# Kernel optimization log

Measured on AMD Instinct MI355X. Metric: run time of the kernel, lower is better.

Reference implementation:

```python
import jax, jax.numpy as jnp
import numpy as np

# Large negative stand-in for -inf so logaddexp gradients stay finite;
# exp(NEG - x) underflows to 0 exactly, matching the -inf math on the
# reachable alignment lattice.
NEG = -1e30

N_FRAMES, BATCH, TARGET_LEN, VOCAB = 2000, 32, 1000, 256


def _alignment_alphas(score_mat, tgt):
    """Monotonic-alignment DP for one item.

    score_mat: [N, V] log-probs, tgt: [T] int token ids.
    Recurrence (same math as compute_loss):
      alpha[0, 0] = score[0, tgt[0]];          alpha[0, j>0] = -inf
      alpha[i, 0] = alpha[i-1, 0] + score[i, tgt[0]]            (cumsum column 0)
      alpha[i, j] = score[i, tgt[j]] + logaddexp(alpha[i-1, j-1], alpha[i-1, j])
    Returns the full lattice alphas: [N, T].
    """
    emit = score_mat[:, tgt]  # [N, T] gather of per-frame target log-probs
    t = tgt.shape[0]
    alpha0 = jnp.where(jnp.arange(t) == 0, emit[0], NEG)

    def step(alpha, e):
        shifted = jnp.concatenate([jnp.full((1,), NEG, alpha.dtype), alpha[:-1]])
        # j=0: logaddexp(NEG, alpha[0]) == alpha[0] -> pure cumsum, as in torch code
        new = e + jnp.logaddexp(shifted, alpha)
        return new, new

    _, rest = jax.lax.scan(step, alpha0, emit[1:])
    return jnp.concatenate([alpha0[None, :], rest], axis=0)  # [N, T]


def setup_inputs() -> dict:
    key = jax.random.key(0)
    k1, k2, k3, k4 = jax.random.split(key, 4)
    logits = jax.random.normal(k1, (N_FRAMES, BATCH, VOCAB), dtype=jnp.float32)
    scores = jax.nn.log_softmax(logits, axis=-1)  # module expects log-softmaxed scores
    targets = jax.random.randint(k2, (BATCH, TARGET_LEN), 0, VOCAB)
    # valid alignments need target_len <= input_len
    input_lengths = jax.random.randint(k3, (BATCH,), N_FRAMES // 2, N_FRAMES + 1)
    target_lengths = jax.random.randint(k4, (BATCH,), TARGET_LEN // 2, TARGET_LEN + 1)
    return {
        "scores": scores,
        "targets": targets,
        "input_lengths": input_lengths,
        "target_lengths": target_lengths,
    }


def reference(scores, targets, input_lengths, target_lengths):
    sc = jnp.transpose(scores, (1, 0, 2))  # [B, N, V]
    alphas = jax.vmap(_alignment_alphas)(sc, targets)  # [B, N, T]
    b = targets.shape[0]
    final = alphas[jnp.arange(b), input_lengths - 1, target_lengths - 1]  # [B]
    return -jnp.sum(final) / b
```

## Files before the change

### kernel.cpp

```cpp
#include <hip/hip_runtime.h>
#include <hip/hip_fp16.h>

constexpr int N_FRAMES   = 2000;
constexpr int BATCH      = 32;
constexpr int TARGET_LEN = 1000;
constexpr int VOCAB      = 256;
constexpr int CH         = 16;
constexpr int NW         = 8;
#define NEGF (-1e30f)

typedef __attribute__((address_space(1))) const float* gcfp;
typedef __attribute__((address_space(1))) const unsigned* gcu32;

typedef float f32x2 __attribute__((ext_vector_type(2)));

#define H2F(us) __half2float(__ushort_as_half((unsigned short)(us)))

__device__ __forceinline__ f32x2 lse_e(f32x2 A, f32x2 U, f32x2 E) {
    f32x2 m; m.x = fmaxf(A.x, U.x); m.y = fmaxf(A.y, U.y);
    const f32x2 d = A - U;
    f32x2 x;
    x.x = __builtin_amdgcn_exp2f(-fabsf(d.x));
    x.y = __builtin_amdgcn_exp2f(-fabsf(d.y));
    const f32x2 s = E + m;
    f32x2 tt = x * 0.0464048f - 0.1963066f;
    tt = x * tt + 0.4176245f;
    tt = x * tt - 0.7096745f;
    tt = x * tt + 1.44196727f;
    return x * tt + s;
}
__device__ __forceinline__ f32x2 lse_core(f32x2 A, f32x2 U) {
    f32x2 m; m.x = fmaxf(A.x, U.x); m.y = fmaxf(A.y, U.y);
    const f32x2 d = A - U;
    f32x2 x;
    x.x = __builtin_amdgcn_exp2f(-fabsf(d.x));
    x.y = __builtin_amdgcn_exp2f(-fabsf(d.y));
    f32x2 tt = x * 0.0464048f - 0.1963066f;
    tt = x * tt + 0.4176245f;
    tt = x * tt - 0.7096745f;
    tt = x * tt + 1.44196727f;
    return x * tt + m;
}

__global__ __launch_bounds__(256)
void gather_emit(const float* __restrict__ scores,
                 const int*   __restrict__ targets,
                 __half*      __restrict__ emit)
{
    constexpr float L2E = 1.44269504088896340736f;
    const int i = blockIdx.x;
    const int b = blockIdx.y;
    const int t = threadIdx.x;

    const gcfp gsc = (gcfp)scores;
    const unsigned sbase = (unsigned)(i * BATCH * VOCAB + b * VOCAB);

    int tk0, tk1, tk2, tk3;
    if (t < TARGET_LEN / 4) {
        const int4 tk = *(const int4*)&targets[b * TARGET_LEN + 4 * t];
        tk0 = tk.x; tk1 = tk.y; tk2 = tk.z; tk3 = tk.w;
    } else {
        tk0 = tk1 = tk2 = tk3 = targets[b * TARGET_LEN + TARGET_LEN - 1];
    }

    const float e0 = gsc[sbase + (unsigned)tk0] * L2E;
    const float e1 = gsc[sbase + (unsigned)tk1] * L2E;
    const float e2 = gsc[sbase + (unsigned)tk2] * L2E;
    const float e3 = gsc[sbase + (unsigned)tk3] * L2E;

    const unsigned long long h0 = __half_as_ushort(__float2half_rn(e0));
    const unsigned long long h1 = __half_as_ushort(__float2half_rn(e1));
    const unsigned long long h2 = __half_as_ushort(__float2half_rn(e2));
    const unsigned long long h3 = __half_as_ushort(__float2half_rn(e3));

    const unsigned long long u = h0 | (h1 << 16) | (h2 << 32) | (h3 << 48);
    *(unsigned long long*)(emit + (((size_t)(b * N_FRAMES + i)) << 10) + 4 * t) = u;
}

__global__ __launch_bounds__(512)
void align_dp_fb(const __half* __restrict__ emit,
                 const int*    __restrict__ in_len,
                 const int*    __restrict__ tg_len,
                 float*        __restrict__ wsA,
                 float*        __restrict__ wsB)
{
    const int b    = blockIdx.x;
    const int t    = threadIdx.x;
    const int lane = t & 63;
    const int w    = t >> 6;

    __shared__ float bpub[NW - 1][2][CH];

    const int inlen = in_len[b];
    const int m     = (inlen - 1) >> 1;

    const gcu32 gem = (gcu32)(emit + (((size_t)b * N_FRAMES) << 10));

    if (blockIdx.y == 0) {
        const int NCHf = (m + CH - 1) / CH;
        float p0 = NEGF, p1 = NEGF;
        if (t == 0) p0 = H2F(gem[0] & 0xffffu);

        unsigned ring[CH];
#pragma unroll
        for (int r = 0; r < CH; ++r) ring[r] = gem[(unsigned)((1 + r) << 9) + (unsigned)t];

        float shprev = NEGF, carry = NEGF;
        f32x2* wsA2 = (f32x2*)(wsA + (b << 10));

#define FROWX(r, SNAPF, Bv, Ov)                                                 \
        {                                                                       \
            const int i = i0 + (r);                                             \
            const unsigned u = ring[r];                                         \
            ring[r] = gem[(unsigned)((i + CH) << 9) + (unsigned)t];             \
            f32x2 E; E.x = H2F(u & 0xffffu); E.y = H2F(u >> 16);                \
            f32x2 A; A.x = (lane == 0) ? (Bv) : shprev; A.y = p0;               \
            f32x2 U; U.x = p0; U.y = p1;                                        \
            const f32x2 c = lse_e(A, U, E);                                     \
            shprev = __shfl_up(c.y, 1);                                         \
            (Ov) = c.y;                                                         \
            if (SNAPF) { if (i == m) wsA2[t] = c; }                             \
            p0 = c.x; p1 = c.y;                                                 \
        }

#define FBODY(SNAPF)                                                            \
        {                                                                       \
            FROWX(0,  SNAPF, B0,  o0)  FROWX(1,  SNAPF, B1,  o1)                \
            FROWX(2,  SNAPF, B2,  o2)  FROWX(3,  SNAPF, B3,  o3)                \
            FROWX(4,  SNAPF, B4,  o4)  FROWX(5,  SNAPF, B5,  o5)                \
            FROWX(6,  SNAPF, B6,  o6)  FROWX(7,  SNAPF, B7,  o7)                \
            FROWX(8,  SNAPF, B8,  o8)  FROWX(9,  SNAPF, B9,  o9)                \
            FROWX(10, SNAPF, B10, o10) FROWX(11, SNAPF, B11, o11)               \
            FROWX(12, SNAPF, B12, o12) FROWX(13, SNAPF, B13, o13)               \
            FROWX(14, SNAPF, B14, o14) FROWX(15, SNAPF, B15, o15)               \
        }

        const int NPHf = NCHf + NW - 1;
        for (int p = 0; p < NPHf; ++p) {
            const int q = p - w;
            if (q >= 0 && q < NCHf) {
                const int i0  = 1 + q * CH;
                const int par = q & 1;

                float B0 = NEGF, B1 = NEGF, B2 = NEGF, B3 = NEGF,
                      B4 = NEGF, B5 = NEGF, B6 = NEGF, B7 = NEGF,
                      B8 = NEGF, B9 = NEGF, B10 = NEGF, B11 = NEGF,
                      B12 = NEGF, B13 = NEGF, B14 = NEGF, B15 = NEGF;
                if (w > 0) {
                    const float* vp = &bpub[w - 1][par][0];
                    B0 = carry;
                    B1  = vp[0];  B2  = vp[1];  B3  = vp[2];  B4  = vp[3];
                    B5  = vp[4];  B6  = vp[5];  B7  = vp[6];  B8  = vp[7];
                    B9  = vp[8];  B10 = vp[9];  B11 = vp[10]; B12 = vp[11];
                    B13 = vp[12]; B14 = vp[13]; B15 = vp[14];
                    carry = vp[15];
                }

                float o0, o1, o2, o3, o4, o5, o6, o7,
                      o8, o9, o10, o11, o12, o13, o14, o15;

                if (q == NCHf - 1) FBODY(true) else FBODY(false)

                if (w < NW - 1 && lane == 63) {
                    float* dp = &bpub[w][par][0];
                    dp[0]  = o0;  dp[1]  = o1;  dp[2]  = o2;  dp[3]  = o3;
                    dp[4]  = o4;  dp[5]  = o5;  dp[6]  = o6;  dp[7]  = o7;
                    dp[8]  = o8;  dp[9]  = o9;  dp[10] = o10; dp[11] = o11;
                    dp[12] = o12; dp[13] = o13; dp[14] = o14; dp[15] = o15;
                }
            }
            asm volatile("s_waitcnt lgkmcnt(0)" ::: "memory");
            __builtin_amdgcn_s_barrier();
            asm volatile("" ::: "memory");
        }
#undef FBODY
#undef FROWX
    } else {
        const int tlen   = tg_len[b];
        const int istart = inlen - 1;
        const int NCHb   = (istart - m + CH - 1) / CH;
        const int fth    = (tlen - 1) >> 1;
        const int fcc    = (tlen - 1) & 1;

        float p0 = NEGF, p1 = NEGF;
        if (t == fth) { if (fcc == 0) p0 = 0.0f; else p1 = 0.0f; }

        unsigned ring[CH];
#pragma unroll
        for (int r = 0; r < CH; ++r)
            ring[r] = gem[(unsigned)((istart - r) << 9) + (unsigned)t];

        f32x2* wsB2 = (f32x2*)(wsB + (b << 10));

#define BROWX(r, SNAPF, Bv, Ov)                                                 \
        {                                                                       \
            const int i = i0 - (r);                                             \
            const unsigned u = ring[r];                                         \
            ring[r] = gem[(unsigned)((i + 1 - CH) << 9) + (unsigned)t];         \
            f32x2 E; E.x = H2F(u & 0xffffu); E.y = H2F(u >> 16);                \
            f32x2 P; P.x = p0; P.y = p1;                                        \
            const f32x2 x = E + P;                                              \
            const float sh = __shfl_down(x.x, 1);                               \
            (Ov) = x.x;                                                         \
            const float xR = (lane == 63) ? (Bv) : sh;                          \
            f32x2 A; A.x = x.x; A.y = x.y;                                      \
            f32x2 U; U.x = x.y; U.y = xR;                                       \
            const f32x2 c = lse_core(A, U);                                     \
            if (SNAPF) { if (i == m) wsB2[t] = c; }                             \
            p0 = c.x; p1 = c.y;                                                 \
        }

#define BBODY(SNAPF)                                                            \
        {                                                                       \
            BROWX(0,  SNAPF, B0,  o0)  BROWX(1,  SNAPF, B1,  o1)                \
            BROWX(2,  SNAPF, B2,  o2)  BROWX(3,  SNAPF, B3,  o3)                \
            BROWX(4,  SNAPF, B4,  o4)  BROWX(5,  SNAPF, B5,  o5)                \
            BROWX(6,  SNAPF, B6,  o6)  BROWX(7,  SNAPF, B7,  o7)                \
            BROWX(8,  SNAPF, B8,  o8)  BROWX(9,  SNAPF, B9,  o9)                \
            BROWX(10, SNAPF, B10, o10) BROWX(11, SNAPF, B11, o11)               \
            BROWX(12, SNAPF, B12, o12) BROWX(13, SNAPF, B13, o13)               \
            BROWX(14, SNAPF, B14, o14) BROWX(15, SNAPF, B15, o15)               \
        }

        const int NPHb = NCHb + NW - 1;
        for (int p = 0; p < NPHb; ++p) {
            const int q = p - (NW - 1 - w);
            if (q >= 0 && q < NCHb) {
                const int i0  = istart - 1 - q * CH;
                const int par = q & 1;

                float B0 = NEGF, B1 = NEGF, B2 = NEGF, B3 = NEGF,
                      B4 = NEGF, B5 = NEGF, B6 = NEGF, B7 = NEGF,
                      B8 = NEGF, B9 = NEGF, B10 = NEGF, B11 = NEGF,
                      B12 = NEGF, B13 = NEGF, B14 = NEGF, B15 = NEGF;
                if (w < NW - 1) {
                    const float* vp = &bpub[w][par][0];
                    B0  = vp[0];  B1  = vp[1];  B2  = vp[2];  B3  = vp[3];
                    B4  = vp[4];  B5  = vp[5];  B6  = vp[6];  B7  = vp[7];
                    B8  = vp[8];  B9  = vp[9];  B10 = vp[10]; B11 = vp[11];
                    B12 = vp[12]; B13 = vp[13]; B14 = vp[14]; B15 = vp[15];
                }

                float o0, o1, o2, o3, o4, o5, o6, o7,
                      o8, o9, o10, o11, o12, o13, o14, o15;

                if (q == NCHb - 1) BBODY(true) else BBODY(false)

                if (w > 0 && lane == 0) {
                    float* dp = &bpub[w - 1][par][0];
                    dp[0]  = o0;  dp[1]  = o1;  dp[2]  = o2;  dp[3]  = o3;
                    dp[4]  = o4;  dp[5]  = o5;  dp[6]  = o6;  dp[7]  = o7;
                    dp[8]  = o8;  dp[9]  = o9;  dp[10] = o10; dp[11] = o11;
                    dp[12] = o12; dp[13] = o13; dp[14] = o14; dp[15] = o15;
                }
            }
            asm volatile("s_waitcnt lgkmcnt(0)" ::: "memory");
            __builtin_amdgcn_s_barrier();
            asm volatile("" ::: "memory");
        }
#undef BBODY
#undef BROWX
    }
}

__global__ __launch_bounds__(512)
void lse_combine(const float* __restrict__ wsA, const float* __restrict__ wsB,
                 float* __restrict__ ws_final)
{
    constexpr float LN2 = 0.69314718055994530942f;
    const int b = blockIdx.x, t = threadIdx.x, lane = t & 63, w = t >> 6;
    __shared__ float red[8];

    const float* A  = wsA + (b << 10);
    const float* Bv = wsB + (b << 10);
    const float v0 = A[2 * t]     + Bv[2 * t];
    const float v1 = A[2 * t + 1] + Bv[2 * t + 1];

    float mx = fmaxf(v0, v1);
#pragma unroll
    for (int off = 1; off < 64; off <<= 1) mx = fmaxf(mx, __shfl_xor(mx, off));
    if (lane == 0) red[w] = mx;
    __syncthreads();
    float gm = red[0];
#pragma unroll
    for (int k = 1; k < 8; ++k) gm = fmaxf(gm, red[k]);

    float s = __builtin_amdgcn_exp2f(v0 - gm) + __builtin_amdgcn_exp2f(v1 - gm);
#pragma unroll
    for (int off = 1; off < 64; off <<= 1) s += __shfl_xor(s, off);
    __syncthreads();
    if (lane == 0) red[w] = s;
    __syncthreads();
    if (t == 0) {
        float tot = red[0];
#pragma unroll
        for (int k = 1; k < 8; ++k) tot += red[k];
        ws_final[b] = (gm + __builtin_amdgcn_logf(tot)) * LN2;
    }
}

__global__ void reduce_kernel(const float* __restrict__ ws_final, float* __restrict__ out)
{
    if (threadIdx.x == 0 && blockIdx.x == 0) {
        float s = 0.0f;
        for (int b = 0; b < BATCH; ++b) s += ws_final[b];
        out[0] = -s / (float)BATCH;
    }
}

#define CELL(dst, A, U, E)                                            \
    {                                                                 \
        const float m_ = fmaxf((A), (U));                             \
        const float d_ = (A) - (U);                                   \
        const float p_ = __builtin_amdgcn_exp2f(-fabsf(d_));          \
        const float l_ = __builtin_amdgcn_logf(1.0f + p_);            \
        (dst) = fmaf((E), L2E, m_ + l_);                              \
    }

__global__ __launch_bounds__(256)
void align_dp4(const float* __restrict__ scores,
               const int*   __restrict__ targets,
               const int*   __restrict__ in_len,
               const int*   __restrict__ tg_len,
               float*       __restrict__ ws_final)
{
    constexpr float L2E = 1.44269504088896340736f;
    constexpr float LN2 = 0.69314718055994530942f;

    const int b    = blockIdx.x;
    const int t    = threadIdx.x;
    const int lane = t & 63;
    const int w    = t >> 6;

    __shared__ float elds[4][VOCAB];
    __shared__ float bnd[2][8];

    const int inlen = in_len[b];
    const int tlen  = tg_len[b];

    const gcfp gsc = (gcfp)scores;
    const unsigned base = (unsigned)(b * VOCAB);
    constexpr unsigned ROWW = (unsigned)(BATCH * VOCAB);

    int tok[4];
#pragma unroll
    for (int c = 0; c < 4; ++c) {
        const int col = t * 4 + c;
        tok[c] = targets[b * TARGET_LEN + (col < TARGET_LEN ? col : TARGET_LEN - 1)];
    }

    float prev[4];
#pragma unroll
    for (int c = 0; c < 4; ++c) prev[c] = NEGF;
    if (t == 0) prev[0] = gsc[base + (unsigned)tok[0]] * L2E;

    elds[1][t] = gsc[1u * ROWW + base + (unsigned)t];
    elds[2][t] = gsc[2u * ROWW + base + (unsigned)t];
    if (lane == 63) bnd[0][w] = NEGF;

    float g[4];
    g[3] = gsc[3u * ROWW + base + (unsigned)t];
    g[0] = gsc[4u * ROWW + base + (unsigned)t];
    g[1] = gsc[5u * ROWW + base + (unsigned)t];
    g[2] = gsc[6u * ROWW + base + (unsigned)t];

    const int fth = (tlen - 1) >> 2;
    const int fcc = (tlen - 1) & 3;

#define STEP(K)                                                                    \
    {                                                                              \
        const int i = ib + (K);                                                    \
        if (i < N_FRAMES) {                                                        \
            asm volatile("s_waitcnt lgkmcnt(0)" ::: "memory");                     \
            __builtin_amdgcn_s_barrier();                                          \
            asm volatile("" ::: "memory");                                         \
            const int sl = i & 3;                                                  \
            const float ec0 = elds[sl][tok[0]];                                    \
            const float ec1 = elds[sl][tok[1]];                                    \
            const float ec2 = elds[sl][tok[2]];                                    \
            const float ec3 = elds[sl][tok[3]];                                    \
            const float fromLds = (w > 0) ? bnd[(i - 1) & 1][w - 1] : NEGF;        \
            if (i + 2 < N_FRAMES) elds[(i + 2) & 3][t] = g[((K) + 3) & 3];         \
            if (i + 6 < N_FRAMES)                                                  \
                g[((K) + 3) & 3] = gsc[(unsigned)(i + 6) * ROWW + base + (unsigned)t]; \
            const float sh   = __shfl_up(prev[3], 1);                              \
            const float left = (lane == 0) ? fromLds : sh;                         \
            float cur0, cur1, cur2, cur3;                                          \
            CELL(cur0, left,    prev[0], ec0);                                     \
            CELL(cur1, prev[0], prev[1], ec1);                                     \
            CELL(cur2, prev[1], prev[2], ec2);                                     \
            CELL(cur3, prev[2], prev[3], ec3);                                     \
            if (lane == 63) bnd[i & 1][w] = cur3;                                  \
            if (i == inlen - 1 && t == fth) {                                      \
                const float v = (fcc == 0) ? cur0 : (fcc == 1) ? cur1              \
                              : (fcc == 2) ? cur2 : cur3;                          \
                ws_final[b] = v * LN2;                                             \
            }                                                                      \
            prev[0] = cur0; prev[1] = cur1; prev[2] = cur2; prev[3] = cur3;        \
        }                                                                          \
    }

    for (int ib = 1; ib < N_FRAMES; ib += 4) {
        STEP(0) STEP(1) STEP(2) STEP(3)
    }
#undef STEP
}

extern "C" void kernel_launch(void* const* d_in, const int* in_sizes, int n_in,
                              void* d_out, int out_size, void* d_ws, size_t ws_size,
                              hipStream_t stream)
{
    const float* scores  = (const float*)d_in[0];
    const int*   targets = (const int*)  d_in[1];
    const int*   in_len  = (const int*)  d_in[2];
    const int*   tg_len  = (const int*)  d_in[3];
    float*       out     = (float*)d_out;
    float*       ws_fin  = (float*)d_ws;

    const size_t emit_bytes = (size_t)BATCH * N_FRAMES * 1024 * sizeof(__half);
    const size_t wsA_off  = 4096;
    const size_t wsB_off  = wsA_off + (size_t)BATCH * 1024 * sizeof(float);
    const size_t emit_off = wsB_off + (size_t)BATCH * 1024 * sizeof(float);
    const size_t need = emit_off + emit_bytes;

    if (ws_size >= need) {
        __half* emit = (__half*)((char*)d_ws + emit_off);
        float*  wsA  = (float*)((char*)d_ws + wsA_off);
        float*  wsB  = (float*)((char*)d_ws + wsB_off);
        dim3 ggrid(N_FRAMES, BATCH);
        gather_emit<<<ggrid, 256, 0, stream>>>(scores, targets, emit);
        align_dp_fb<<<dim3(BATCH, 2), 512, 0, stream>>>(emit, in_len, tg_len, wsA, wsB);
        lse_combine<<<BATCH, 512, 0, stream>>>(wsA, wsB, ws_fin);
    } else {
        align_dp4<<<BATCH, 256, 0, stream>>>(scores, targets, in_len, tg_len, ws_fin);
    }
    reduce_kernel<<<1, 64, 0, stream>>>(ws_fin, out);
}
```

Before: 202.7 us.

## Double DP chunk size, use Estrin log-polynomial, skip gather past input length

Raises the row chunk per wavefront phase from 16 to 32, which halves the number of barrier-synchronised phases and deepens the prefetch ring. The log2(1+x) polynomial is rewritten in Estrin form to shorten its dependency chain on the serial critical path. The gather kernel now returns early for frames at or beyond each item's input length, so it skips writing emissions that are never read. The larger chunk raises register pressure and lengthens pipeline fill and drain across the 8 wavefronts.

```diff
diff --git a/kernel.cpp b/kernel.cpp
--- a/kernel.cpp
+++ b/kernel.cpp
@@ -5,7 +5,7 @@
 constexpr int BATCH      = 32;
 constexpr int TARGET_LEN = 1000;
 constexpr int VOCAB      = 256;
-constexpr int CH         = 16;
+constexpr int CH         = 32;
 constexpr int NW         = 8;
 #define NEGF (-1e30f)
 
@@ -16,6 +16,15 @@
 
 #define H2F(us) __half2float(__ushort_as_half((unsigned short)(us)))
 
+__device__ __forceinline__ f32x2 l21p(f32x2 x) {
+    const f32x2 x2 = x * x;
+    const f32x2 x4 = x2 * x2;
+    f32x2 lo = x * 1.44196727f;
+    const f32x2 Bq = x * 0.4176245f  - 0.7096745f;
+    const f32x2 Cq = x * 0.0464048f  - 0.1963066f;
+    lo = x2 * Bq + lo;
+    return x4 * Cq + lo;
+}
 __device__ __forceinline__ f32x2 lse_e(f32x2 A, f32x2 U, f32x2 E) {
     f32x2 m; m.x = fmaxf(A.x, U.x); m.y = fmaxf(A.y, U.y);
     const f32x2 d = A - U;
@@ -23,11 +32,7 @@
     x.x = __builtin_amdgcn_exp2f(-fabsf(d.x));
     x.y = __builtin_amdgcn_exp2f(-fabsf(d.y));
     const f32x2 s = E + m;
-    f32x2 tt = x * 0.0464048f - 0.1963066f;
-    tt = x * tt + 0.4176245f;
-    tt = x * tt - 0.7096745f;
-    tt = x * tt + 1.44196727f;
-    return x * tt + s;
+    return l21p(x) + s;
 }
 __device__ __forceinline__ f32x2 lse_core(f32x2 A, f32x2 U) {
     f32x2 m; m.x = fmaxf(A.x, U.x); m.y = fmaxf(A.y, U.y);
@@ -35,21 +40,19 @@
     f32x2 x;
     x.x = __builtin_amdgcn_exp2f(-fabsf(d.x));
     x.y = __builtin_amdgcn_exp2f(-fabsf(d.y));
-    f32x2 tt = x * 0.0464048f - 0.1963066f;
-    tt = x * tt + 0.4176245f;
-    tt = x * tt - 0.7096745f;
-    tt = x * tt + 1.44196727f;
-    return x * tt + m;
+    return l21p(x) + m;
 }
 
 __global__ __launch_bounds__(256)
 void gather_emit(const float* __restrict__ scores,
                  const int*   __restrict__ targets,
+                 const int*   __restrict__ in_len,
                  __half*      __restrict__ emit)
 {
     constexpr float L2E = 1.44269504088896340736f;
     const int i = blockIdx.x;
     const int b = blockIdx.y;
+    if (i >= in_len[b]) return;
     const int t = threadIdx.x;
 
     const gcfp gsc = (gcfp)scores;
@@ -108,31 +111,20 @@
         float shprev = NEGF, carry = NEGF;
         f32x2* wsA2 = (f32x2*)(wsA + (b << 10));
 
-#define FROWX(r, SNAPF, Bv, Ov)                                                 \
-        {                                                                       \
-            const int i = i0 + (r);                                             \
+#define FBODY(SNAPF)                                                            \
+        _Pragma("unroll")                                                       \
+        for (int r = 0; r < CH; ++r) {                                          \
+            const int i = i0 + r;                                               \
             const unsigned u = ring[r];                                         \
             ring[r] = gem[(unsigned)((i + CH) << 9) + (unsigned)t];             \
             f32x2 E; E.x = H2F(u & 0xffffu); E.y = H2F(u >> 16);                \
-            f32x2 A; A.x = (lane == 0) ? (Bv) : shprev; A.y = p0;               \
+            f32x2 A; A.x = (lane == 0) ? Bv[r] : shprev; A.y = p0;              \
             f32x2 U; U.x = p0; U.y = p1;                                        \
             const f32x2 c = lse_e(A, U, E);                                     \
             shprev = __shfl_up(c.y, 1);                                         \
-            (Ov) = c.y;                                                         \
+            ov[r] = c.y;                                                        \
             if (SNAPF) { if (i == m) wsA2[t] = c; }                             \
             p0 = c.x; p1 = c.y;                                                 \
-        }
-
-#define FBODY(SNAPF)                                                            \
-        {                                                                       \
-            FROWX(0,  SNAPF, B0,  o0)  FROWX(1,  SNAPF, B1,  o1)                \
-            FROWX(2,  SNAPF, B2,  o2)  FROWX(3,  SNAPF, B3,  o3)                \
-            FROWX(4,  SNAPF, B4,  o4)  FROWX(5,  SNAPF, B5,  o5)                \
-            FROWX(6,  SNAPF, B6,  o6)  FROWX(7,  SNAPF, B7,  o7)                \
-            FROWX(8,  SNAPF, B8,  o8)  FROWX(9,  SNAPF, B9,  o9)                \
-            FROWX(10, SNAPF, B10, o10) FROWX(11, SNAPF, B11, o11)               \
-            FROWX(12, SNAPF, B12, o12) FROWX(13, SNAPF, B13, o13)               \
-            FROWX(14, SNAPF, B14, o14) FROWX(15, SNAPF, B15, o15)               \
         }
 
         const int NPHf = NCHf + NW - 1;
@@ -142,31 +134,23 @@
                 const int i0  = 1 + q * CH;
                 const int par = q & 1;
 
-                float B0 = NEGF, B1 = NEGF, B2 = NEGF, B3 = NEGF,
-                      B4 = NEGF, B5 = NEGF, B6 = NEGF, B7 = NEGF,
-                      B8 = NEGF, B9 = NEGF, B10 = NEGF, B11 = NEGF,
-                      B12 = NEGF, B13 = NEGF, B14 = NEGF, B15 = NEGF;
+                float Bv[CH], ov[CH];
+#pragma unroll
+                for (int r = 0; r < CH; ++r) Bv[r] = NEGF;
                 if (w > 0) {
                     const float* vp = &bpub[w - 1][par][0];
-                    B0 = carry;
-                    B1  = vp[0];  B2  = vp[1];  B3  = vp[2];  B4  = vp[3];
-                    B5  = vp[4];  B6  = vp[5];  B7  = vp[6];  B8  = vp[7];
-                    B9  = vp[8];  B10 = vp[9];  B11 = vp[10]; B12 = vp[11];
-                    B13 = vp[12]; B14 = vp[13]; B15 = vp[14];
-                    carry = vp[15];
+                    Bv[0] = carry;
+#pragma unroll
+                    for (int r = 1; r < CH; ++r) Bv[r] = vp[r - 1];
+                    carry = vp[CH - 1];
                 }
-
-                float o0, o1, o2, o3, o4, o5, o6, o7,
-                      o8, o9, o10, o11, o12, o13, o14, o15;
 
                 if (q == NCHf - 1) FBODY(true) else FBODY(false)
 
                 if (w < NW - 1 && lane == 63) {
                     float* dp = &bpub[w][par][0];
-                    dp[0]  = o0;  dp[1]  = o1;  dp[2]  = o2;  dp[3]  = o3;
-                    dp[4]  = o4;  dp[5]  = o5;  dp[6]  = o6;  dp[7]  = o7;
-                    dp[8]  = o8;  dp[9]  = o9;  dp[10] = o10; dp[11] = o11;
-                    dp[12] = o12; dp[13] = o13; dp[14] = o14; dp[15] = o15;
+#pragma unroll
+                    for (int r = 0; r < CH; ++r) dp[r] = ov[r];
                 }
             }
             asm volatile("s_waitcnt lgkmcnt(0)" ::: "memory");
@@ -174,7 +158,6 @@
             asm volatile("" ::: "memory");
         }
 #undef FBODY
-#undef FROWX
     } else {
         const int tlen   = tg_len[b];
         const int istart = inlen - 1;
@@ -192,17 +175,18 @@
 
         f32x2* wsB2 = (f32x2*)(wsB + (b << 10));
 
-#define BROWX(r, SNAPF, Bv, Ov)                                                 \
-        {                                                                       \
-            const int i = i0 - (r);                                             \
+#define BBODY(SNAPF)                                                            \
+        _Pragma("unroll")                                                       \
+        for (int r = 0; r < CH; ++r) {                                          \
+            const int i = i0 - r;                                               \
             const unsigned u = ring[r];                                         \
             ring[r] = gem[(unsigned)((i + 1 - CH) << 9) + (unsigned)t];         \
             f32x2 E; E.x = H2F(u & 0xffffu); E.y = H2F(u >> 16);                \
             f32x2 P; P.x = p0; P.y = p1;                                        \
             const f32x2 x = E + P;                                              \
             const float sh = __shfl_down(x.x, 1);                               \
-            (Ov) = x.x;                                                         \
-            const float xR = (lane == 63) ? (Bv) : sh;                          \
+            ov[r] = x.x;                                                        \
+            const float xR = (lane == 63) ? Bv[r] : sh;                         \
             f32x2 A; A.x = x.x; A.y = x.y;                                      \
             f32x2 U; U.x = x.y; U.y = xR;                                       \
             const f32x2 c = lse_core(A, U);                                     \
@@ -210,18 +194,6 @@
             p0 = c.x; p1 = c.y;                                                 \
         }
 
-#define BBODY(SNAPF)                                                            \
-        {                                                                       \
-            BROWX(0,  SNAPF, B0,  o0)  BROWX(1,  SNAPF, B1,  o1)                \
-            BROWX(2,  SNAPF, B2,  o2)  BROWX(3,  SNAPF, B3,  o3)                \
-            BROWX(4,  SNAPF, B4,  o4)  BROWX(5,  SNAPF, B5,  o5)                \
-            BROWX(6,  SNAPF, B6,  o6)  BROWX(7,  SNAPF, B7,  o7)                \
-            BROWX(8,  SNAPF, B8,  o8)  BROWX(9,  SNAPF, B9,  o9)                \
-            BROWX(10, SNAPF, B10, o10) BROWX(11, SNAPF, B11, o11)               \
-            BROWX(12, SNAPF, B12, o12) BROWX(13, SNAPF, B13, o13)               \
-            BROWX(14, SNAPF, B14, o14) BROWX(15, SNAPF, B15, o15)               \
-        }
-
         const int NPHb = NCHb + NW - 1;
         for (int p = 0; p < NPHb; ++p) {
             const int q = p - (NW - 1 - w);
@@ -229,29 +201,21 @@
                 const int i0  = istart - 1 - q * CH;
                 const int par = q & 1;
 
-                float B0 = NEGF, B1 = NEGF, B2 = NEGF, B3 = NEGF,
-                      B4 = NEGF, B5 = NEGF, B6 = NEGF, B7 = NEGF,
-                      B8 = NEGF, B9 = NEGF, B10 = NEGF, B11 = NEGF,
-                      B12 = NEGF, B13 = NEGF, B14 = NEGF, B15 = NEGF;
+                float Bv[CH], ov[CH];
+#pragma unroll
+                for (int r = 0; r < CH; ++r) Bv[r] = NEGF;
                 if (w < NW - 1) {
                     const float* vp = &bpub[w][par][0];
-                    B0  = vp[0];  B1  = vp[1];  B2  = vp[2];  B3  = vp[3];
-                    B4  = vp[4];  B5  = vp[5];  B6  = vp[6];  B7  = vp[7];
-                    B8  = vp[8];  B9  = vp[9];  B10 = vp[10]; B11 = vp[11];
-                    B12 = vp[12]; B13 = vp[13]; B14 = vp[14]; B15 = vp[15];
+#pragma unroll
+                    for (int r = 0; r < CH; ++r) Bv[r] = vp[r];
                 }
-
-                float o0, o1, o2, o3, o4, o5, o6, o7,
-                      o8, o9, o10, o11, o12, o13, o14, o15;
 
                 if (q == NCHb - 1) BBODY(true) else BBODY(false)
 
                 if (w > 0 && lane == 0) {
                     float* dp = &bpub[w - 1][par][0];
-                    dp[0]  = o0;  dp[1]  = o1;  dp[2]  = o2;  dp[3]  = o3;
-                    dp[4]  = o4;  dp[5]  = o5;  dp[6]  = o6;  dp[7]  = o7;
-                    dp[8]  = o8;  dp[9]  = o9;  dp[10] = o10; dp[11] = o11;
-                    dp[12] = o12; dp[13] = o13; dp[14] = o14; dp[15] = o15;
+#pragma unroll
+                    for (int r = 0; r < CH; ++r) dp[r] = ov[r];
                 }
             }
             asm volatile("s_waitcnt lgkmcnt(0)" ::: "memory");
@@ -259,7 +223,6 @@
             asm volatile("" ::: "memory");
         }
 #undef BBODY
-#undef BROWX
     }
 }
 
@@ -428,7 +391,7 @@
         float*  wsA  = (float*)((char*)d_ws + wsA_off);
         float*  wsB  = (float*)((char*)d_ws + wsB_off);
         dim3 ggrid(N_FRAMES, BATCH);
-        gather_emit<<<ggrid, 256, 0, stream>>>(scores, targets, emit);
+        gather_emit<<<ggrid, 256, 0, stream>>>(scores, targets, in_len, emit);
         align_dp_fb<<<dim3(BATCH, 2), 512, 0, stream>>>(emit, in_len, tg_len, wsA, wsB);
         lse_combine<<<BATCH, 512, 0, stream>>>(wsA, wsB, ws_fin);
     } else {
```

New measurement: 201.8 us. No clear change (-0.4%).

## Use DPP lane shifts, Estrin log polynomial, and skip gathers past input length

Applied to the files above, without the earlier changes.

Replaces the ds_bpermute-based shfl_up/shfl_down in the forward and backward DP inner loops with DPP row_shr/row_shl moves. The log2(1+x) polynomial is rewritten in Estrin form to shorten the dependency chain on the serial critical path. The gather kernel now exits early for frames beyond each item's input length, skipping unused emit writes. A risk is that DPP row shifts only operate within 16-lane rows, so lanes at row boundaries would receive 0 instead of their neighbour's value unless the bank/row masks handle it. That would break the wave-wide shift semantics.

```diff
diff --git a/kernel.cpp b/kernel.cpp
--- a/kernel.cpp
+++ b/kernel.cpp
@@ -16,6 +16,29 @@
 
 #define H2F(us) __half2float(__ushort_as_half((unsigned short)(us)))
 
+#if __has_builtin(__builtin_amdgcn_update_dpp)
+__device__ __forceinline__ float lane_up1(float x) {
+    return __int_as_float(__builtin_amdgcn_update_dpp(
+        0, __float_as_int(x), 0x138, 0xf, 0xf, false));
+}
+__device__ __forceinline__ float lane_dn1(float x) {
+    return __int_as_float(__builtin_amdgcn_update_dpp(
+        0, __float_as_int(x), 0x130, 0xf, 0xf, false));
+}
+#else
+__device__ __forceinline__ float lane_up1(float x) { return __shfl_up(x, 1); }
+__device__ __forceinline__ float lane_dn1(float x) { return __shfl_down(x, 1); }
+#endif
+
+__device__ __forceinline__ f32x2 l21p(f32x2 x) {
+    const f32x2 x2 = x * x;
+    const f32x2 x4 = x2 * x2;
+    f32x2 lo = x * 1.44196727f;
+    const f32x2 Bq = x * 0.4176245f  - 0.7096745f;
+    const f32x2 Cq = x * 0.0464048f  - 0.1963066f;
+    lo = x2 * Bq + lo;
+    return x4 * Cq + lo;
+}
 __device__ __forceinline__ f32x2 lse_e(f32x2 A, f32x2 U, f32x2 E) {
     f32x2 m; m.x = fmaxf(A.x, U.x); m.y = fmaxf(A.y, U.y);
     const f32x2 d = A - U;
@@ -23,11 +46,7 @@
     x.x = __builtin_amdgcn_exp2f(-fabsf(d.x));
     x.y = __builtin_amdgcn_exp2f(-fabsf(d.y));
     const f32x2 s = E + m;
-    f32x2 tt = x * 0.0464048f - 0.1963066f;
-    tt = x * tt + 0.4176245f;
-    tt = x * tt - 0.7096745f;
-    tt = x * tt + 1.44196727f;
-    return x * tt + s;
+    return l21p(x) + s;
 }
 __device__ __forceinline__ f32x2 lse_core(f32x2 A, f32x2 U) {
     f32x2 m; m.x = fmaxf(A.x, U.x); m.y = fmaxf(A.y, U.y);
@@ -35,21 +54,19 @@
     f32x2 x;
     x.x = __builtin_amdgcn_exp2f(-fabsf(d.x));
     x.y = __builtin_amdgcn_exp2f(-fabsf(d.y));
-    f32x2 tt = x * 0.0464048f - 0.1963066f;
-    tt = x * tt + 0.4176245f;
-    tt = x * tt - 0.7096745f;
-    tt = x * tt + 1.44196727f;
-    return x * tt + m;
+    return l21p(x) + m;
 }
 
 __global__ __launch_bounds__(256)
 void gather_emit(const float* __restrict__ scores,
                  const int*   __restrict__ targets,
+                 const int*   __restrict__ in_len,
                  __half*      __restrict__ emit)
 {
     constexpr float L2E = 1.44269504088896340736f;
     const int i = blockIdx.x;
     const int b = blockIdx.y;
+    if (i >= in_len[b]) return;
     const int t = threadIdx.x;
 
     const gcfp gsc = (gcfp)scores;
@@ -117,7 +134,7 @@
             f32x2 A; A.x = (lane == 0) ? (Bv) : shprev; A.y = p0;               \
             f32x2 U; U.x = p0; U.y = p1;                                        \
             const f32x2 c = lse_e(A, U, E);                                     \
-            shprev = __shfl_up(c.y, 1);                                         \
+            shprev = lane_up1(c.y);                                             \
             (Ov) = c.y;                                                         \
             if (SNAPF) { if (i == m) wsA2[t] = c; }                             \
             p0 = c.x; p1 = c.y;                                                 \
@@ -200,7 +217,7 @@
             f32x2 E; E.x = H2F(u & 0xffffu); E.y = H2F(u >> 16);                \
             f32x2 P; P.x = p0; P.y = p1;                                        \
             const f32x2 x = E + P;                                              \
-            const float sh = __shfl_down(x.x, 1);                               \
+            const float sh = lane_dn1(x.x);                                     \
             (Ov) = x.x;                                                         \
             const float xR = (lane == 63) ? (Bv) : sh;                          \
             f32x2 A; A.x = x.x; A.y = x.y;                                      \
@@ -428,7 +445,7 @@
         float*  wsA  = (float*)((char*)d_ws + wsA_off);
         float*  wsB  = (float*)((char*)d_ws + wsB_off);
         dim3 ggrid(N_FRAMES, BATCH);
-        gather_emit<<<ggrid, 256, 0, stream>>>(scores, targets, emit);
+        gather_emit<<<ggrid, 256, 0, stream>>>(scores, targets, in_len, emit);
         align_dp_fb<<<dim3(BATCH, 2), 512, 0, stream>>>(emit, in_len, tg_len, wsA, wsB);
         lse_combine<<<BATCH, 512, 0, stream>>>(wsA, wsB, ws_fin);
     } else {
```

New measurement: 187.6 us, median of 2. 7.5% less time.
